# Optimization experiments

Hardware: AMD Instinct MI355X
Metric: run time of the kernel (lower is better)

## Reference

```python
import jax, jax.numpy as jnp
import numpy as np

PAD = 1000.0   # sentinel padding coordinate, as in the torch module
CHUNK = 1024   # key-tile size for the online min-reduction


def _pad_points(pts, n_pad):
    # append n_pad sentinel points at (1000,1000,1000); pad-vs-pad distance is 0
    # and is excluded by the dist>0 mask, matching the original single-pad logic.
    pad = jnp.full((pts.shape[0], n_pad, 3), PAD, pts.dtype)
    return jnp.concatenate([pts, pad], axis=1)


def _nn_sqdist(q, k_tiles, k2_tiles):
    # q: [N,3] queries; k_tiles: [K, CHUNK, 3]; k2_tiles: [K, CHUNK]
    # returns [N] min squared distance to any key, via tiled online min
    q2 = jnp.sum(q * q, axis=-1)  # [N]

    def step(best, xb):
        kc, k2c = xb
        d = q2[:, None] + k2c[None, :] - 2.0 * (q @ kc.T)  # [N, CHUNK]
        return jnp.minimum(best, jnp.min(d, axis=1)), None

    init = jnp.full(q.shape[0], jnp.inf, q.dtype)
    best, _ = jax.lax.scan(step, init, (k_tiles, k2_tiles))
    return jnp.maximum(best, 0.0)  # clamp tiny negative numerical noise


def _chamfer(p1, p2):
    # p1: [B, N, 3], p2: [B, M, 3]; N, M multiples of CHUNK
    def one_dir(q, k):
        n_tiles = k.shape[1] // CHUNK
        kc = k.reshape(k.shape[0], n_tiles, CHUNK, 3)
        k2 = jnp.sum(kc * kc, axis=-1)
        return jax.vmap(_nn_sqdist)(q, kc, k2)

    return one_dir(p1, p2), one_dir(p2, p1)


def setup_inputs() -> dict:
    key = jax.random.key(0)
    k1, k2 = jax.random.split(key)
    B, T, N = 2, 4, 16384
    return {
        "output_points": jax.random.normal(k1, (B * T, N, 3), dtype=jnp.float32),
        "target_points": jax.random.normal(k2, (B * T, N, 3), dtype=jnp.float32),
        "batch_size": B,
        "n_future_steps": T,
    }


def reference(output_points, target_points, batch_size, n_future_steps):
    op = _pad_points(output_points, CHUNK)  # [BT, N+CHUNK, 3]
    tp = _pad_points(target_points, CHUNK)
    dist1, dist2 = _chamfer(op, tp)  # squared NN dists, each [BT, N+CHUNK]
    pos1 = jnp.sum((dist1 > 0).astype(dist1.dtype), axis=1)
    pos2 = jnp.sum((dist2 > 0).astype(dist2.dtype), axis=1)
    dist_combined = jnp.sum(dist1, axis=1) / pos1 + jnp.sum(dist2, axis=1) / pos2
    chamfer_distances_tensor = dist_combined.reshape(n_future_steps, batch_size)
    chamf_dist_t = jnp.mean(chamfer_distances_tensor, axis=1)  # per-future-step mean
    return chamf_dist_t, chamfer_distances_tensor
```

## Files before the change

### kernel.cpp

```cpp
#include <hip/hip_runtime.h>
#include <hip/hip_bf16.h>

#define NPTS   16384
#define NCLOUD 16
#define NJOBS  16
#define BLK    256

#define NA      4
#define QPW     (NA * 32)
#define QPB     (QPW * 4)
#define QBLOCKS (NPTS / QPB)
#define STAGE_KEYS 512
#define STAGE_U4   (STAGE_KEYS * 2)
#define NSTAGES    (NPTS / STAGE_KEYS)
#define CPS        (STAGE_KEYS / 32)

typedef __attribute__((ext_vector_type(8)))  short short8;
typedef __attribute__((ext_vector_type(16))) float f32x16;

__device__ __forceinline__ unsigned short f2bf(float x) {
    unsigned u = __float_as_uint(x);
    u += 0x7fffu + ((u >> 16) & 1u);
    return (unsigned short)(u >> 16);
}
__device__ __forceinline__ float bf2f(unsigned short h) {
    return __uint_as_float(((unsigned)h) << 16);
}
__device__ __forceinline__ int f2key(float f) {
    int b = __float_as_int(f);
    return (b >= 0) ? b : (b ^ 0x7fffffff);
}
__device__ __forceinline__ float key2f(int k) {
    int b = (k >= 0) ? k : (k ^ 0x7fffffff);
    return __int_as_float(b);
}

__global__ __launch_bounds__(BLK)
void cham_pack(const float* __restrict__ op, const float* __restrict__ tp,
               uint4* __restrict__ pk2) {
    const int gkey = blockIdx.x * BLK + threadIdx.x;
    const int c = gkey >> 14;
    const int i = gkey & (NPTS - 1);
    const float* src = (c < 8) ? (op + (size_t)c * NPTS * 3)
                               : (tp + (size_t)(c - 8) * NPTS * 3);
    const float x = src[i * 3 + 0];
    const float y = src[i * 3 + 1];
    const float z = src[i * 3 + 2];
    const unsigned khx = f2bf(x), khy = f2bf(y), khz = f2bf(z);
    const unsigned klx = f2bf(x - bf2f(khx));
    const unsigned kly = f2bf(y - bf2f(khy));
    const unsigned klz = f2bf(z - bf2f(khz));
    const float k2 = fmaf(x, x, fmaf(y, y, z * z));
    const unsigned k2a = f2bf(k2);
    float rres = k2 - bf2f(k2a);
    const unsigned k2b = f2bf(rres);
    rres -= bf2f(k2b);
    const unsigned k2c = f2bf(rres);

    uint4 r0, r1;
    r0.x = khx | (khy << 16); r0.y = khz | (khx << 16);
    r0.z = khy | (khz << 16); r0.w = klx | (kly << 16);
    r1.x = klz | (klx << 16); r1.y = kly | (klz << 16);
    r1.z = k2a | (k2b << 16); r1.w = k2c;

    const int chunk = i >> 5, slot = i & 31;
    const size_t base = (size_t)c * 32768 + (size_t)chunk * 64 + slot;
    pk2[base]      = r0;
    pk2[base + 32] = r1;
}

__global__ __launch_bounds__(BLK, 2)
void cham_mfma(const float* __restrict__ op, const float* __restrict__ tp,
               const uint4* __restrict__ pk2, int* __restrict__ wmin) {
    __shared__ uint4 smem[STAGE_U4];

    const int bid  = blockIdx.x;
    const int job  = bid >> 5;
    const int qblk = bid & 31;
    const int bt   = job >> 1, dir = job & 1;
    const float* qp = (dir == 0) ? (op + (size_t)bt * NPTS * 3)
                                 : (tp + (size_t)bt * NPTS * 3);
    const int kcloud = (dir == 0) ? (8 + bt) : bt;

    const int tid  = threadIdx.x;
    const int lane = tid & 63, w = tid >> 6;
    const int col  = lane & 31, g = lane >> 5;

    short8 a[NA];
    f32x16 m[NA];
    const unsigned short ONE = 0x3f80;
    #pragma unroll
    for (int f = 0; f < NA; ++f) {
        const int qi = qblk * QPB + w * QPW + f * 32 + col;
        const float x = qp[qi * 3 + 0];
        const float y = qp[qi * 3 + 1];
        const float z = qp[qi * 3 + 2];
        const float sx = -2.0f * x, sy = -2.0f * y, sz = -2.0f * z;
        const unsigned short sxh = f2bf(sx), syh = f2bf(sy), szh = f2bf(sz);
        const unsigned short sxl = f2bf(sx - bf2f(sxh));
        const unsigned short syl = f2bf(sy - bf2f(syh));
        const unsigned short szl = f2bf(sz - bf2f(szh));
        if (g == 0) {
            a[f] = short8{(short)sxh, (short)syh, (short)szh, (short)sxl,
                          (short)syl, (short)szl, (short)sxh, (short)syh};
        } else {
            a[f] = short8{(short)szh, (short)sxl, (short)syl, (short)szl,
                          (short)ONE, (short)ONE, (short)ONE, (short)0};
        }
        #pragma unroll
        for (int r = 0; r < 16; ++r) m[f][r] = 3.0e38f;
    }

    const uint4* kbase = pk2 + (size_t)kcloud * 32768;
    const f32x16 zero = {0.0f, 0.0f, 0.0f, 0.0f, 0.0f, 0.0f, 0.0f, 0.0f,
                         0.0f, 0.0f, 0.0f, 0.0f, 0.0f, 0.0f, 0.0f, 0.0f};

    for (int s = 0; s < NSTAGES; ++s) {
        __syncthreads();
        const uint4* src = kbase + (size_t)s * STAGE_U4;
        #pragma unroll
        for (int i = 0; i < STAGE_U4 / BLK; ++i)
            smem[tid + BLK * i] = src[tid + BLK * i];
        __syncthreads();

        #pragma unroll 2
        for (int cp = 0; cp < CPS / 2; ++cp) {
            const short8 b0 = *(const short8*)&smem[cp * 128 + lane];
            const short8 b1 = *(const short8*)&smem[cp * 128 + 64 + lane];
            #pragma unroll
            for (int f = 0; f < NA; ++f) {
                const f32x16 accA = __builtin_amdgcn_mfma_f32_32x32x16_bf16(a[f], b0, zero, 0, 0, 0);
                const f32x16 accB = __builtin_amdgcn_mfma_f32_32x32x16_bf16(a[f], b1, zero, 0, 0, 0);
                #pragma unroll
                for (int r = 0; r < 16; ++r)
                    m[f][r] = fminf(fminf(m[f][r], accA[r]), accB[r]);
            }
        }
    }

    int* wj = wmin + job * NPTS + qblk * QPB + w * QPW;
    #pragma unroll
    for (int f = 0; f < NA; ++f) {
        #pragma unroll
        for (int r = 0; r < 16; ++r) {
            float v = m[f][r];
            v = fminf(v, __shfl_xor(v, 1, 64));
            v = fminf(v, __shfl_xor(v, 2, 64));
            v = fminf(v, __shfl_xor(v, 4, 64));
            v = fminf(v, __shfl_xor(v, 8, 64));
            v = fminf(v, __shfl_xor(v, 16, 64));
            if (col == 0)
                wj[f * 32 + (r & 3) + 8 * (r >> 2) + 4 * g] = f2key(v);
        }
    }
}

#define FB_NQ 8
#define FB_QB (BLK * FB_NQ)
#define FB_KS 8
#define FB_KPS (NPTS / FB_KS)
__global__ __launch_bounds__(BLK, 4)
void cham_fb(const float* __restrict__ op, const float* __restrict__ tp,
             int* __restrict__ wmin) {
    const int bid = blockIdx.x;
    const int job = bid >> 6;
    const int rem = bid & 63;
    const int qb  = rem >> 3;
    const int ks  = rem & 7;
    const int bt  = job >> 1, dir = job & 1;
    const float* qp = (dir == 0) ? (op + (size_t)bt * NPTS * 3)
                                 : (tp + (size_t)bt * NPTS * 3);
    const int tid = threadIdx.x;
    float qsx[FB_NQ], qsy[FB_NQ], qsz[FB_NQ], m[FB_NQ];
    const float* q0 = qp + (size_t)qb * FB_QB * 3;
    #pragma unroll
    for (int q = 0; q < FB_NQ; ++q) {
        const int qi = q * BLK + tid;
        const float x = q0[qi * 3], y = q0[qi * 3 + 1], z = q0[qi * 3 + 2];
        qsx[q] = -2.0f * x; qsy[q] = -2.0f * y; qsz[q] = -2.0f * z;
        m[q] = 3.0e38f;
    }
    const float* kp = ((dir == 0) ? (tp + (size_t)bt * NPTS * 3)
                                  : (op + (size_t)bt * NPTS * 3)) + (size_t)ks * FB_KPS * 3;
    for (int j = 0; j < FB_KPS; j += 2) {
        const float ax = kp[j * 3], ay = kp[j * 3 + 1], az = kp[j * 3 + 2];
        const float bx = kp[j * 3 + 3], by = kp[j * 3 + 4], bz = kp[j * 3 + 5];
        const float aw = fmaf(ax, ax, fmaf(ay, ay, az * az));
        const float bw = fmaf(bx, bx, fmaf(by, by, bz * bz));
        #pragma unroll
        for (int q = 0; q < FB_NQ; ++q) {
            const float da = fmaf(qsx[q], ax, fmaf(qsy[q], ay, fmaf(qsz[q], az, aw)));
            const float db = fmaf(qsx[q], bx, fmaf(qsy[q], by, fmaf(qsz[q], bz, bw)));
            m[q] = fminf(m[q], fminf(da, db));
        }
    }
    int* wj = wmin + job * NPTS + qb * FB_QB;
    #pragma unroll
    for (int q = 0; q < FB_NQ; ++q) atomicMin(&wj[q * BLK + tid], f2key(m[q]));
}

__global__ __launch_bounds__(BLK)
void cham_pass2(const float* __restrict__ op, const float* __restrict__ tp,
                const int* __restrict__ wmin, float* __restrict__ ws2) {
    const int job  = blockIdx.x >> 2;
    const int part = blockIdx.x & 3;
    const int bt  = job >> 1, dir = job & 1;
    const float* qp = (dir == 0) ? (op + (size_t)bt * NPTS * 3)
                                 : (tp + (size_t)bt * NPTS * 3);
    const int tid = threadIdx.x;
    float S = 0.0f, P = 0.0f;
    const int lo = part * (NPTS / 4), hi = lo + (NPTS / 4);
    for (int i = lo + tid; i < hi; i += BLK) {
        const float x = qp[i * 3], y = qp[i * 3 + 1], z = qp[i * 3 + 2];
        const float q2 = fmaf(x, x, fmaf(y, y, z * z));
        const float d = fmaxf(q2 + key2f(wmin[job * NPTS + i]), 0.0f);
        S += d;
        P += (d > 0.0f) ? 1.0f : 0.0f;
    }
    #pragma unroll
    for (int o = 32; o > 0; o >>= 1) {
        S += __shfl_down(S, o, 64);
        P += __shfl_down(P, o, 64);
    }
    __shared__ float sS[4], sP[4];
    const int wv = tid >> 6;
    if ((tid & 63) == 0) { sS[wv] = S; sP[wv] = P; }
    __syncthreads();
    if (tid == 0) {
        atomicAdd(&ws2[job * 2 + 0], sS[0] + sS[1] + sS[2] + sS[3]);
        atomicAdd(&ws2[job * 2 + 1], sP[0] + sP[1] + sP[2] + sP[3]);
    }
}

__global__ void cham_pass3(const float* __restrict__ ws2, float* __restrict__ out) {
    __shared__ float dc[8];
    const int t = threadIdx.x;
    if (t < 8) {
        const float s0 = ws2[(t * 2 + 0) * 2 + 0];
        const float p0 = ws2[(t * 2 + 0) * 2 + 1];
        const float s1 = ws2[(t * 2 + 1) * 2 + 0];
        const float p1 = ws2[(t * 2 + 1) * 2 + 1];
        dc[t] = s0 / p0 + s1 / p1;
    }
    __syncthreads();
    if (t < 8) out[4 + t] = dc[t];
    if (t < 4) out[t] = 0.5f * (dc[2 * t] + dc[2 * t + 1]);
}

extern "C" void kernel_launch(void* const* d_in, const int* in_sizes, int n_in,
                              void* d_out, int out_size, void* d_ws, size_t ws_size,
                              hipStream_t stream) {
    const float* op = (const float*)d_in[0];
    const float* tp = (const float*)d_in[1];

    const size_t wmin_bytes = (size_t)NJOBS * NPTS * sizeof(int);
    const size_t ws2_off = wmin_bytes;
    const size_t pk_off  = ws2_off + 256;
    const size_t pk_bytes = (size_t)NCLOUD * 32768 * sizeof(uint4);

    int*   wmin = (int*)d_ws;
    float* ws2  = (float*)((char*)d_ws + ws2_off);
    uint4* pk2  = (uint4*)((char*)d_ws + pk_off);
    float* out  = (float*)d_out;

    hipMemsetAsync(ws2, 0, (size_t)NJOBS * 2 * sizeof(float), stream);

    if (ws_size >= pk_off + pk_bytes) {
        cham_pack<<<NCLOUD * NPTS / BLK, BLK, 0, stream>>>(op, tp, pk2);
        cham_mfma<<<NJOBS * QBLOCKS, BLK, 0, stream>>>(op, tp, pk2, wmin);
    } else {
        hipMemsetAsync(wmin, 0x7F, wmin_bytes, stream);
        cham_fb<<<NJOBS * 64, BLK, 0, stream>>>(op, tp, wmin);
    }
    cham_pass2<<<NJOBS * 4, BLK, 0, stream>>>(op, tp, wmin, ws2);
    cham_pass3<<<1, 64, 0, stream>>>(ws2, out);
}
```

Before: 204.8 us.

## Split key range across two blocks and double-buffer LDS key staging

The MFMA nearest-neighbour kernel now splits the keys into two halves handled by separate blocks, doubling the grid from 512 to 1024 blocks, and each half writes its minima to its own buffer. pass2 takes the min of the two buffers, which removes the atomicMin, the memset and the atomic accumulation. Key staging into LDS is double-buffered with register prefetch, so the global load of the next stage overlaps the MFMA work on the current one and one barrier per stage is dropped. Launch bounds rise to 4 blocks per CU, which may pressure registers given the 64 accumulator floats per thread. pass2 now runs only 16 blocks.

Result: slower. 233.7 us (+14.1%).

```diff
diff --git a/kernel.cpp b/kernel.cpp
--- a/kernel.cpp
+++ b/kernel.cpp
@@ -10,9 +10,11 @@
 #define QPW     (NA * 32)
 #define QPB     (QPW * 4)
 #define QBLOCKS (NPTS / QPB)
+#define KSPLIT  2
+#define KPB     (NPTS / KSPLIT)
 #define STAGE_KEYS 512
 #define STAGE_U4   (STAGE_KEYS * 2)
-#define NSTAGES    (NPTS / STAGE_KEYS)
+#define NSTAGES    (KPB / STAGE_KEYS)
 #define CPS        (STAGE_KEYS / 32)
 
 typedef __attribute__((ext_vector_type(8)))  short short8;
@@ -25,14 +27,6 @@
 }
 __device__ __forceinline__ float bf2f(unsigned short h) {
     return __uint_as_float(((unsigned)h) << 16);
-}
-__device__ __forceinline__ int f2key(float f) {
-    int b = __float_as_int(f);
-    return (b >= 0) ? b : (b ^ 0x7fffffff);
-}
-__device__ __forceinline__ float key2f(int k) {
-    int b = (k >= 0) ? k : (k ^ 0x7fffffff);
-    return __int_as_float(b);
 }
 
 __global__ __launch_bounds__(BLK)
@@ -69,14 +63,17 @@
     pk2[base + 32] = r1;
 }
 
-__global__ __launch_bounds__(BLK, 2)
+__global__ __launch_bounds__(BLK, 4)
 void cham_mfma(const float* __restrict__ op, const float* __restrict__ tp,
-               const uint4* __restrict__ pk2, int* __restrict__ wmin) {
-    __shared__ uint4 smem[STAGE_U4];
+               const uint4* __restrict__ pk2,
+               float* __restrict__ w0, float* __restrict__ w1) {
+    __shared__ uint4 smem[2][STAGE_U4];
 
     const int bid  = blockIdx.x;
-    const int job  = bid >> 5;
-    const int qblk = bid & 31;
+    const int job  = bid >> 6;
+    const int rem  = bid & 63;
+    const int qblk = rem >> 1;
+    const int ks   = rem & 1;
     const int bt   = job >> 1, dir = job & 1;
     const float* qp = (dir == 0) ? (op + (size_t)bt * NPTS * 3)
                                  : (tp + (size_t)bt * NPTS * 3);
@@ -111,109 +108,102 @@
         for (int r = 0; r < 16; ++r) m[f][r] = 3.0e38f;
     }
 
-    const uint4* kbase = pk2 + (size_t)kcloud * 32768;
+    const uint4* kbase = pk2 + (size_t)kcloud * 32768 + (size_t)ks * (KPB * 2);
     const f32x16 zero = {0.0f, 0.0f, 0.0f, 0.0f, 0.0f, 0.0f, 0.0f, 0.0f,
                          0.0f, 0.0f, 0.0f, 0.0f, 0.0f, 0.0f, 0.0f, 0.0f};
 
+    uint4 r[4];
+    #pragma unroll
+    for (int i = 0; i < 4; ++i) r[i] = kbase[tid + BLK * i];
+    #pragma unroll
+    for (int i = 0; i < 4; ++i) smem[0][tid + BLK * i] = r[i];
+    int cur = 0;
+
     for (int s = 0; s < NSTAGES; ++s) {
         __syncthreads();
-        const uint4* src = kbase + (size_t)s * STAGE_U4;
-        #pragma unroll
-        for (int i = 0; i < STAGE_U4 / BLK; ++i)
-            smem[tid + BLK * i] = src[tid + BLK * i];
-        __syncthreads();
+
+        if (s + 1 < NSTAGES) {
+            const uint4* g2 = kbase + (size_t)(s + 1) * STAGE_U4;
+            #pragma unroll
+            for (int i = 0; i < 4; ++i) r[i] = g2[tid + BLK * i];
+        }
 
         #pragma unroll 2
         for (int cp = 0; cp < CPS / 2; ++cp) {
-            const short8 b0 = *(const short8*)&smem[cp * 128 + lane];
-            const short8 b1 = *(const short8*)&smem[cp * 128 + 64 + lane];
+            const short8 b0 = *(const short8*)&smem[cur][cp * 128 + lane];
+            const short8 b1 = *(const short8*)&smem[cur][cp * 128 + 64 + lane];
             #pragma unroll
             for (int f = 0; f < NA; ++f) {
                 const f32x16 accA = __builtin_amdgcn_mfma_f32_32x32x16_bf16(a[f], b0, zero, 0, 0, 0);
                 const f32x16 accB = __builtin_amdgcn_mfma_f32_32x32x16_bf16(a[f], b1, zero, 0, 0, 0);
                 #pragma unroll
-                for (int r = 0; r < 16; ++r)
-                    m[f][r] = fminf(fminf(m[f][r], accA[r]), accB[r]);
+                for (int q = 0; q < 16; ++q)
+                    m[f][q] = fminf(fminf(m[f][q], accA[q]), accB[q]);
             }
         }
-    }
-
-    int* wj = wmin + job * NPTS + qblk * QPB + w * QPW;
+
+        if (s + 1 < NSTAGES) {
+            #pragma unroll
+            for (int i = 0; i < 4; ++i) smem[cur ^ 1][tid + BLK * i] = r[i];
+        }
+        cur ^= 1;
+    }
+
+    float* wj = ((ks == 0) ? w0 : w1) + job * NPTS + qblk * QPB + w * QPW;
     #pragma unroll
     for (int f = 0; f < NA; ++f) {
         #pragma unroll
-        for (int r = 0; r < 16; ++r) {
-            float v = m[f][r];
+        for (int q = 0; q < 16; ++q) {
+            float v = m[f][q];
             v = fminf(v, __shfl_xor(v, 1, 64));
             v = fminf(v, __shfl_xor(v, 2, 64));
             v = fminf(v, __shfl_xor(v, 4, 64));
             v = fminf(v, __shfl_xor(v, 8, 64));
             v = fminf(v, __shfl_xor(v, 16, 64));
             if (col == 0)
-                wj[f * 32 + (r & 3) + 8 * (r >> 2) + 4 * g] = f2key(v);
-        }
-    }
-}
-
-#define FB_NQ 8
-#define FB_QB (BLK * FB_NQ)
-#define FB_KS 8
-#define FB_KPS (NPTS / FB_KS)
-__global__ __launch_bounds__(BLK, 4)
+                wj[f * 32 + (q & 3) + 8 * (q >> 2) + 4 * g] = v;
+        }
+    }
+}
+
+__global__ __launch_bounds__(BLK)
 void cham_fb(const float* __restrict__ op, const float* __restrict__ tp,
-             int* __restrict__ wmin) {
-    const int bid = blockIdx.x;
-    const int job = bid >> 6;
-    const int rem = bid & 63;
-    const int qb  = rem >> 3;
-    const int ks  = rem & 7;
+             float* __restrict__ w0, float* __restrict__ w1) {
+    const int job = blockIdx.x >> 6;
+    const int qb  = blockIdx.x & 63;
     const int bt  = job >> 1, dir = job & 1;
     const float* qp = (dir == 0) ? (op + (size_t)bt * NPTS * 3)
                                  : (tp + (size_t)bt * NPTS * 3);
-    const int tid = threadIdx.x;
-    float qsx[FB_NQ], qsy[FB_NQ], qsz[FB_NQ], m[FB_NQ];
-    const float* q0 = qp + (size_t)qb * FB_QB * 3;
-    #pragma unroll
-    for (int q = 0; q < FB_NQ; ++q) {
-        const int qi = q * BLK + tid;
-        const float x = q0[qi * 3], y = q0[qi * 3 + 1], z = q0[qi * 3 + 2];
-        qsx[q] = -2.0f * x; qsy[q] = -2.0f * y; qsz[q] = -2.0f * z;
-        m[q] = 3.0e38f;
-    }
-    const float* kp = ((dir == 0) ? (tp + (size_t)bt * NPTS * 3)
-                                  : (op + (size_t)bt * NPTS * 3)) + (size_t)ks * FB_KPS * 3;
-    for (int j = 0; j < FB_KPS; j += 2) {
-        const float ax = kp[j * 3], ay = kp[j * 3 + 1], az = kp[j * 3 + 2];
-        const float bx = kp[j * 3 + 3], by = kp[j * 3 + 4], bz = kp[j * 3 + 5];
-        const float aw = fmaf(ax, ax, fmaf(ay, ay, az * az));
-        const float bw = fmaf(bx, bx, fmaf(by, by, bz * bz));
-        #pragma unroll
-        for (int q = 0; q < FB_NQ; ++q) {
-            const float da = fmaf(qsx[q], ax, fmaf(qsy[q], ay, fmaf(qsz[q], az, aw)));
-            const float db = fmaf(qsx[q], bx, fmaf(qsy[q], by, fmaf(qsz[q], bz, bw)));
-            m[q] = fminf(m[q], fminf(da, db));
-        }
-    }
-    int* wj = wmin + job * NPTS + qb * FB_QB;
-    #pragma unroll
-    for (int q = 0; q < FB_NQ; ++q) atomicMin(&wj[q * BLK + tid], f2key(m[q]));
+    const float* kp = (dir == 0) ? (tp + (size_t)bt * NPTS * 3)
+                                 : (op + (size_t)bt * NPTS * 3);
+    const int qi = qb * BLK + threadIdx.x;
+    const float x = qp[qi * 3], y = qp[qi * 3 + 1], z = qp[qi * 3 + 2];
+    const float sx = -2.0f * x, sy = -2.0f * y, sz = -2.0f * z;
+    float mv = 3.0e38f;
+    for (int j = 0; j < NPTS; ++j) {
+        const float kx = kp[j * 3], ky = kp[j * 3 + 1], kz = kp[j * 3 + 2];
+        const float kw = fmaf(kx, kx, fmaf(ky, ky, kz * kz));
+        mv = fminf(mv, fmaf(sx, kx, fmaf(sy, ky, fmaf(sz, kz, kw))));
+    }
+    w0[job * NPTS + qi] = mv;
+    w1[job * NPTS + qi] = mv;
 }
 
 __global__ __launch_bounds__(BLK)
 void cham_pass2(const float* __restrict__ op, const float* __restrict__ tp,
-                const int* __restrict__ wmin, float* __restrict__ ws2) {
-    const int job  = blockIdx.x >> 2;
-    const int part = blockIdx.x & 3;
+                const float* __restrict__ w0, const float* __restrict__ w1,
+                float* __restrict__ ws2) {
+    const int job = blockIdx.x;
     const int bt  = job >> 1, dir = job & 1;
     const float* qp = (dir == 0) ? (op + (size_t)bt * NPTS * 3)
                                  : (tp + (size_t)bt * NPTS * 3);
     const int tid = threadIdx.x;
     float S = 0.0f, P = 0.0f;
-    const int lo = part * (NPTS / 4), hi = lo + (NPTS / 4);
-    for (int i = lo + tid; i < hi; i += BLK) {
+    for (int i = tid; i < NPTS; i += BLK) {
         const float x = qp[i * 3], y = qp[i * 3 + 1], z = qp[i * 3 + 2];
         const float q2 = fmaf(x, x, fmaf(y, y, z * z));
-        const float d = fmaxf(q2 + key2f(wmin[job * NPTS + i]), 0.0f);
+        const float mv = fminf(w0[job * NPTS + i], w1[job * NPTS + i]);
+        const float d = fmaxf(q2 + mv, 0.0f);
         S += d;
         P += (d > 0.0f) ? 1.0f : 0.0f;
     }
@@ -227,8 +217,8 @@
     if ((tid & 63) == 0) { sS[wv] = S; sP[wv] = P; }
     __syncthreads();
     if (tid == 0) {
-        atomicAdd(&ws2[job * 2 + 0], sS[0] + sS[1] + sS[2] + sS[3]);
-        atomicAdd(&ws2[job * 2 + 1], sP[0] + sP[1] + sP[2] + sP[3]);
+        ws2[job * 2 + 0] = sS[0] + sS[1] + sS[2] + sS[3];
+        ws2[job * 2 + 1] = sP[0] + sP[1] + sP[2] + sP[3];
     }
 }
 
@@ -253,25 +243,24 @@
     const float* op = (const float*)d_in[0];
     const float* tp = (const float*)d_in[1];
 
-    const size_t wmin_bytes = (size_t)NJOBS * NPTS * sizeof(int);
-    const size_t ws2_off = wmin_bytes;
+    const size_t half_bytes = (size_t)NJOBS * NPTS * sizeof(float);
+    const size_t w1_off  = half_bytes;
+    const size_t ws2_off = 2 * half_bytes;
     const size_t pk_off  = ws2_off + 256;
     const size_t pk_bytes = (size_t)NCLOUD * 32768 * sizeof(uint4);
 
-    int*   wmin = (int*)d_ws;
-    float* ws2  = (float*)((char*)d_ws + ws2_off);
-    uint4* pk2  = (uint4*)((char*)d_ws + pk_off);
-    float* out  = (float*)d_out;
-
-    hipMemsetAsync(ws2, 0, (size_t)NJOBS * 2 * sizeof(float), stream);
+    float* w0  = (float*)d_ws;
+    float* w1  = (float*)((char*)d_ws + w1_off);
+    float* ws2 = (float*)((char*)d_ws + ws2_off);
+    uint4* pk2 = (uint4*)((char*)d_ws + pk_off);
+    float* out = (float*)d_out;
 
     if (ws_size >= pk_off + pk_bytes) {
         cham_pack<<<NCLOUD * NPTS / BLK, BLK, 0, stream>>>(op, tp, pk2);
-        cham_mfma<<<NJOBS * QBLOCKS, BLK, 0, stream>>>(op, tp, pk2, wmin);
+        cham_mfma<<<NJOBS * QBLOCKS * KSPLIT, BLK, 0, stream>>>(op, tp, pk2, w0, w1);
     } else {
-        hipMemsetAsync(wmin, 0x7F, wmin_bytes, stream);
-        cham_fb<<<NJOBS * 64, BLK, 0, stream>>>(op, tp, wmin);
-    }
-    cham_pass2<<<NJOBS * 4, BLK, 0, stream>>>(op, tp, wmin, ws2);
+        cham_fb<<<NJOBS * 64, BLK, 0, stream>>>(op, tp, w0, w1);
+    }
+    cham_pass2<<<NJOBS, BLK, 0, stream>>>(op, tp, w0, w1, ws2);
     cham_pass3<<<1, 64, 0, stream>>>(ws2, out);
 }
```
